# Kernel tuning notes

Measured on AMD Instinct MI355X. Metric: run time of the kernel, lower is better.

## Reference

```python
import jax, jax.numpy as jnp
import numpy as np

D_MODEL = 2048
NUM_HEADS = 32
NUM_KV_HEADS = 8
HEAD_DIM = D_MODEL // NUM_HEADS
ROPE_BASE = 10000.0


def _rope_cos_sin(T, dtype):
    # standard LLaMA-style RoPE tables, shape (1, 1, T, head_dim)
    half = HEAD_DIM // 2
    inv_freq = 1.0 / (ROPE_BASE ** (jnp.arange(0, half, dtype=jnp.float32) / half))
    pos = jnp.arange(T, dtype=jnp.float32)
    freqs = pos[:, None] * inv_freq[None, :]          # (T, half)
    emb = jnp.concatenate([freqs, freqs], axis=-1)     # (T, head_dim)
    cos = jnp.cos(emb)[None, None].astype(dtype)
    sin = jnp.sin(emb)[None, None].astype(dtype)
    return cos, sin


def _rotate_half(x):
    h = x.shape[-1] // 2
    return jnp.concatenate([-x[..., h:], x[..., :h]], axis=-1)


def setup_inputs() -> dict:
    key = jax.random.key(0)
    ks = jax.random.split(key, 5)
    B, T = 2, 2048
    s = 1.0 / np.sqrt(D_MODEL)
    return {
        "x": jax.random.normal(ks[0], (B, T, D_MODEL), jnp.float32),
        "Wq": jax.random.normal(ks[1], (D_MODEL, D_MODEL), jnp.float32) * s,
        "Wk": jax.random.normal(ks[2], (NUM_KV_HEADS * HEAD_DIM, D_MODEL), jnp.float32) * s,
        "Wv": jax.random.normal(ks[3], (NUM_KV_HEADS * HEAD_DIM, D_MODEL), jnp.float32) * s,
        "Wo": jax.random.normal(ks[4], (D_MODEL, D_MODEL), jnp.float32) * s,
    }


def reference(x, Wq, Wk, Wv, Wo):
    B, T, _ = x.shape
    # projections (torch Linear: y = x @ W.T)
    Q = (x @ Wq.T).reshape(B, T, NUM_HEADS, HEAD_DIM).transpose(0, 2, 1, 3)      # (B,H,T,D)
    K = (x @ Wk.T).reshape(B, T, NUM_KV_HEADS, HEAD_DIM).transpose(0, 2, 1, 3)   # (B,Hkv,T,D)
    V = (x @ Wv.T).reshape(B, T, NUM_KV_HEADS, HEAD_DIM).transpose(0, 2, 1, 3)

    cos, sin = _rope_cos_sin(T, x.dtype)
    Q = Q * cos + _rotate_half(Q) * sin
    K = K * cos + _rotate_half(K) * sin

    # GQA: expand kv heads to query heads
    heads_per_kv = NUM_HEADS // NUM_KV_HEADS
    group_map = jnp.arange(NUM_HEADS) // heads_per_kv
    K_sel = K[:, group_map]  # (B,H,T,D)
    V_sel = V[:, group_map]

    scale = 1.0 / np.sqrt(HEAD_DIM)
    scores = jnp.einsum("bhqd,bhkd->bhqk", Q, K_sel) * scale
    causal = jnp.tril(jnp.ones((T, T), dtype=bool))
    scores = jnp.where(causal, scores, jnp.finfo(scores.dtype).min)
    attn = jax.nn.softmax(scores, axis=-1)
    out = jnp.einsum("bhqk,bhkd->bhqd", attn, V_sel)
    out = out.transpose(0, 2, 1, 3).reshape(B, T, D_MODEL)
    return out @ Wo.T
```

## Files before the change

### kernel.cpp

```cpp
#include <hip/hip_runtime.h>
#include <stdint.h>


typedef unsigned short u16;
typedef __attribute__((ext_vector_type(8))) short short8;
typedef __attribute__((ext_vector_type(4))) float floatx4;

#define T_SEQ 2048
#define DMODEL 2048
#define NHEADS 32
#define KVHEADS 8
#define HDIM 64
#define QK_SCALE 0.1803368801111204f

__device__ __forceinline__ u16 f2bf(float f) {
  uint32_t u = __builtin_bit_cast(uint32_t, f);
  u = (u + 0x7FFFu + ((u >> 16) & 1u)) >> 16;
  return (u16)u;
}
__device__ __forceinline__ float bf2f(u16 h) {
  uint32_t u = ((uint32_t)h) << 16;
  return __builtin_bit_cast(float, u);
}
__device__ __forceinline__ uint32_t cvtpk(float a, float b) {
  uint32_t r;
  asm("v_cvt_pk_bf16_f32 %0, %1, %2" : "=v"(r) : "v"(a), "v"(b));
  return r;
}

__device__ __forceinline__ void gld_lds16(const void* g, void* l) {
  __builtin_amdgcn_global_load_lds(
      (const __attribute__((address_space(1))) unsigned int*)g,
      (__attribute__((address_space(3))) unsigned int*)l, 16, 0, 0);
}

__global__ __launch_bounds__(256) void cvt_kernel(const float* __restrict__ src,
                                                  u16* __restrict__ dst, int n4) {
  int i = blockIdx.x * 256 + threadIdx.x;
  if (i >= n4) return;
  float4 v = ((const float4*)src)[i];
  ushort4 o;
  o.x = f2bf(v.x); o.y = f2bf(v.y); o.z = f2bf(v.z); o.w = f2bf(v.w);
  ((ushort4*)dst)[i] = o;
}

__global__ __launch_bounds__(256) void rope_table_kernel(float* __restrict__ cosT,
                                                         float* __restrict__ sinT) {
  int idx = blockIdx.x * 256 + threadIdx.x;
  int t = idx >> 5, i = idx & 31;
  float invf = 1.0f / powf(10000.0f, (float)i / 32.0f);
  float a = (float)t * invf;
  cosT[idx] = cosf(a);
  sinT[idx] = sinf(a);
}

template <bool OUT_F32>
__global__ __launch_bounds__(256) void gemm_bt(const u16* __restrict__ A,
                                               const u16* __restrict__ Bm,
                                               float* __restrict__ Cf,
                                               u16* __restrict__ Cb,
                                               int M, int N, int K) {
  __shared__ u16 As[128 * 64];
  __shared__ u16 Bs[128 * 64];
  const int tid = threadIdx.x;
  const int lane = tid & 63;
  const int wid = tid >> 6;
  const int wr = wid >> 1, wc = wid & 1;
  const long bm = (long)blockIdx.y * 128;
  const long bn = (long)blockIdx.x * 128;

  floatx4 acc[4][4] = {};

  for (int kt = 0; kt < K; kt += 64) {
#pragma unroll
    for (int c = 0; c < 4; ++c) {
      int g = (wid * 4 + c) * 64 + lane;
      int row = g >> 3, slot = g & 7;
      int ss = slot ^ (row & 7);
      gld_lds16(A + (bm + row) * (long)K + kt + ss * 8, (char*)As + g * 16);
      gld_lds16(Bm + (bn + row) * (long)K + kt + ss * 8, (char*)Bs + g * 16);
    }
    __syncthreads();
#pragma unroll
    for (int ks = 0; ks < 2; ++ks) {
      short8 af[4], bfr[4];
#pragma unroll
      for (int m = 0; m < 4; ++m) {
        int row = wr * 64 + m * 16 + (lane & 15);
        int slot = (ks * 4 + (lane >> 4)) ^ (row & 7);
        af[m] = *(const short8*)((const char*)As + row * 128 + slot * 16);
      }
#pragma unroll
      for (int n = 0; n < 4; ++n) {
        int row = wc * 64 + n * 16 + (lane & 15);
        int slot = (ks * 4 + (lane >> 4)) ^ (row & 7);
        bfr[n] = *(const short8*)((const char*)Bs + row * 128 + slot * 16);
      }
#pragma unroll
      for (int m = 0; m < 4; ++m)
#pragma unroll
        for (int n = 0; n < 4; ++n)
          acc[m][n] = __builtin_amdgcn_mfma_f32_16x16x32_bf16(af[m], bfr[n],
                                                              acc[m][n], 0, 0, 0);
    }
    __syncthreads();
  }
#pragma unroll
  for (int m = 0; m < 4; ++m)
#pragma unroll
    for (int n = 0; n < 4; ++n)
#pragma unroll
      for (int r = 0; r < 4; ++r) {
        long row = bm + wr * 64 + m * 16 + (lane >> 4) * 4 + r;
        long col = bn + wc * 64 + n * 16 + (lane & 15);
        if constexpr (OUT_F32)
          Cf[row * N + col] = acc[m][n][r];
        else
          Cb[row * N + col] = f2bf(acc[m][n][r]);
      }
}

__global__ __launch_bounds__(256) void rope_apply_kernel(
    const u16* __restrict__ QKV, const float* __restrict__ cosT,
    const float* __restrict__ sinT, u16* __restrict__ Qh, u16* __restrict__ Kh) {
  int idx = blockIdx.x * 256 + threadIdx.x;
  int c = idx % 2560;
  int bt = idx / 2560;
  int t = bt & (T_SEQ - 1);
  int b = bt >> 11;
  int hd = c & 63;
  int i = hd & 31;
  float cs = cosT[t * 32 + i];
  float sn = sinT[t * 32 + i];
  long base = (long)bt * 3072;
  float xv = bf2f(QKV[base + c]);
  int pairc = (hd < 32) ? c + 32 : c - 32;
  float xp = bf2f(QKV[base + pairc]);
  float rot = (hd < 32) ? -xp : xp;
  float ov = xv * cs + rot * sn;
  if (c < 2048) {
    int h = c >> 6;
    Qh[((long)(b * NHEADS + h) * T_SEQ + t) * HDIM + hd] = f2bf(ov * QK_SCALE);
  } else {
    int kv = (c - 2048) >> 6;
    Kh[((long)(b * KVHEADS + kv) * T_SEQ + t) * HDIM + hd] = f2bf(ov);
  }
}

__global__ __launch_bounds__(256) void v_transpose_kernel(const u16* __restrict__ QKV,
                                                          u16* __restrict__ Vt) {
  __shared__ u16 tl[64 * 65];
  int blk = blockIdx.x;
  int ttile = blk & 31;
  int kvh = (blk >> 5) & 7;
  int b = blk >> 8;
  int tid = threadIdx.x;
  long bt0 = (long)b * T_SEQ + ttile * 64;
#pragma unroll
  for (int j = 0; j < 2; ++j) {
    int chunk = tid * 2 + j;
    int el = chunk * 8;
    int row = el >> 6, col = el & 63;
    short8 v = *(const short8*)(QKV + (bt0 + row) * 3072 + 2560 + kvh * 64 + col);
#pragma unroll
    for (int k = 0; k < 8; ++k) tl[(col + k) * 65 + row] = (u16)v[k];
  }
  __syncthreads();
#pragma unroll
  for (int j = 0; j < 2; ++j) {
    int chunk = tid * 2 + j;
    int el = chunk * 8;
    int d = el >> 6, t0 = el & 63;
    short8 o;
#pragma unroll
    for (int k = 0; k < 8; ++k) o[k] = (short)tl[d * 65 + t0 + k];
    *(short8*)(Vt + ((long)(b * KVHEADS + kvh) * HDIM + d) * T_SEQ + ttile * 64 + t0) = o;
  }
}

#define ATT_BODY(BUF)                                                          \
  {                                                                            \
    asm volatile("s_waitcnt vmcnt(0)" ::: "memory");                           \
    __builtin_amdgcn_s_barrier();                                              \
    asm volatile("" ::: "memory");                                             \
    if (kt < qb) {                                                             \
      gld_lds16(kg0, (char*)KS + ((BUF ^ 1) * 8192) + ld0);                    \
      gld_lds16(kg1, (char*)KS + ((BUF ^ 1) * 8192) + ld1);                    \
      gld_lds16(vg0, (char*)VS + ((BUF ^ 1) * 8192) + ld0);                    \
      gld_lds16(vg1, (char*)VS + ((BUF ^ 1) * 8192) + ld1);                    \
      kg0 += 4096; kg1 += 4096; vg0 += 64; vg1 += 64;                          \
    }                                                                          \
    floatx4 st[4] = {};                                                        \
    __builtin_amdgcn_s_setprio(1);                                             \
    {                                                                          \
      short8 kf0 = *(const short8*)((const char*)KS + BUF * 8192 + aK0);       \
      short8 kf1 = *(const short8*)((const char*)KS + BUF * 8192 + aK0 + 2048);\
      short8 kf2 = *(const short8*)((const char*)KS + BUF * 8192 + aK0 + 4096);\
      short8 kf3 = *(const short8*)((const char*)KS + BUF * 8192 + aK0 + 6144);\
      st[0] = __builtin_amdgcn_mfma_f32_16x16x32_bf16(kf0, qf0, st[0], 0, 0, 0);\
      st[1] = __builtin_amdgcn_mfma_f32_16x16x32_bf16(kf1, qf0, st[1], 0, 0, 0);\
      st[2] = __builtin_amdgcn_mfma_f32_16x16x32_bf16(kf2, qf0, st[2], 0, 0, 0);\
      st[3] = __builtin_amdgcn_mfma_f32_16x16x32_bf16(kf3, qf0, st[3], 0, 0, 0);\
      kf0 = *(const short8*)((const char*)KS + BUF * 8192 + aK1);              \
      kf1 = *(const short8*)((const char*)KS + BUF * 8192 + aK1 + 2048);       \
      kf2 = *(const short8*)((const char*)KS + BUF * 8192 + aK1 + 4096);       \
      kf3 = *(const short8*)((const char*)KS + BUF * 8192 + aK1 + 6144);       \
      st[0] = __builtin_amdgcn_mfma_f32_16x16x32_bf16(kf0, qf1, st[0], 0, 0, 0);\
      st[1] = __builtin_amdgcn_mfma_f32_16x16x32_bf16(kf1, qf1, st[1], 0, 0, 0);\
      st[2] = __builtin_amdgcn_mfma_f32_16x16x32_bf16(kf2, qf1, st[2], 0, 0, 0);\
      st[3] = __builtin_amdgcn_mfma_f32_16x16x32_bf16(kf3, qf1, st[3], 0, 0, 0);\
    }                                                                          \
    __builtin_amdgcn_s_setprio(0);                                             \
    if (kt == qb) {                                                            \
      _Pragma("unroll") for (int tt = 0; tt < 4; ++tt)                         \
        _Pragma("unroll") for (int r = 0; r < 4; ++r) {                        \
          int tg = kt * 64 + tt * 16 + l4 * 4 + r;                             \
          if (tg > qg) st[tt][r] = -1e30f;                                     \
        }                                                                      \
    }                                                                          \
    float mx0 = fmaxf(fmaxf(st[0][0], st[0][1]), fmaxf(st[0][2], st[0][3]));   \
    float mx1 = fmaxf(fmaxf(st[1][0], st[1][1]), fmaxf(st[1][2], st[1][3]));   \
    float mx2 = fmaxf(fmaxf(st[2][0], st[2][1]), fmaxf(st[2][2], st[2][3]));   \
    float mx3 = fmaxf(fmaxf(st[3][0], st[3][1]), fmaxf(st[3][2], st[3][3]));   \
    float mt = fmaxf(fmaxf(mx0, mx1), fmaxf(mx2, mx3));                        \
    mt = fmaxf(mt, __shfl_xor(mt, 16));                                        \
    mt = fmaxf(mt, __shfl_xor(mt, 32));                                        \
    bool defer = __all(mt - m_run <= 8.0f);                                    \
    float m_use = defer ? m_run : fmaxf(m_run, mt);                            \
    float alpha = defer ? 1.0f : exp2f(m_run - m_use);                         \
    float lsp[4];                                                              \
    _Pragma("unroll") for (int tt = 0; tt < 4; ++tt) {                         \
      float e0 = exp2f(st[tt][0] - m_use);                                     \
      float e1 = exp2f(st[tt][1] - m_use);                                     \
      float e2 = exp2f(st[tt][2] - m_use);                                     \
      float e3 = exp2f(st[tt][3] - m_use);                                     \
      st[tt][0] = e0; st[tt][1] = e1;                                          \
      lsp[tt] = (e0 + e1) + (e2 + e3);                                         \
      uint2 pk;                                                                \
      pk.x = cvtpk(e0, e1);                                                    \
      pk.y = cvtpk(e2, e3);                                                    \
      *(uint2*)((char*)Ps + (pwb ^ (tt << 5))) = pk;                           \
    }                                                                          \
    float lsum = (lsp[0] + lsp[1]) + (lsp[2] + lsp[3]);                        \
    lsum += __shfl_xor(lsum, 16);                                              \
    lsum += __shfl_xor(lsum, 32);                                              \
    l_run = l_run * alpha + lsum;                                              \
    m_run = m_use;                                                             \
    if (!defer) {                                                              \
      float a0 = __shfl(alpha, l4 * 4 + 0);                                    \
      float a1 = __shfl(alpha, l4 * 4 + 1);                                    \
      float a2 = __shfl(alpha, l4 * 4 + 2);                                    \
      float a3 = __shfl(alpha, l4 * 4 + 3);                                    \
      _Pragma("unroll") for (int dd = 0; dd < 4; ++dd) {                       \
        oA[dd][0] *= a0; oA[dd][1] *= a1; oA[dd][2] *= a2; oA[dd][3] *= a3;    \
      }                                                                        \
    }                                                                          \
    asm volatile("s_waitcnt lgkmcnt(0)" ::: "memory");                         \
    __builtin_amdgcn_s_setprio(1);                                             \
    {                                                                          \
      short8 pa = *(const short8*)((const char*)Ps + pr0);                     \
      short8 vb0 = *(const short8*)((const char*)VS + BUF * 8192 + aK0);       \
      short8 vb1 = *(const short8*)((const char*)VS + BUF * 8192 + aK0 + 2048);\
      short8 vb2 = *(const short8*)((const char*)VS + BUF * 8192 + aK0 + 4096);\
      short8 vb3 = *(const short8*)((const char*)VS + BUF * 8192 + aK0 + 6144);\
      oA[0] = __builtin_amdgcn_mfma_f32_16x16x32_bf16(pa, vb0, oA[0], 0, 0, 0);\
      oA[1] = __builtin_amdgcn_mfma_f32_16x16x32_bf16(pa, vb1, oA[1], 0, 0, 0);\
      oA[2] = __builtin_amdgcn_mfma_f32_16x16x32_bf16(pa, vb2, oA[2], 0, 0, 0);\
      oA[3] = __builtin_amdgcn_mfma_f32_16x16x32_bf16(pa, vb3, oA[3], 0, 0, 0);\
      pa = *(const short8*)((const char*)Ps + pr1);                            \
      vb0 = *(const short8*)((const char*)VS + BUF * 8192 + aK1);              \
      vb1 = *(const short8*)((const char*)VS + BUF * 8192 + aK1 + 2048);       \
      vb2 = *(const short8*)((const char*)VS + BUF * 8192 + aK1 + 4096);       \
      vb3 = *(const short8*)((const char*)VS + BUF * 8192 + aK1 + 6144);       \
      oA[0] = __builtin_amdgcn_mfma_f32_16x16x32_bf16(pa, vb0, oA[0], 0, 0, 0);\
      oA[1] = __builtin_amdgcn_mfma_f32_16x16x32_bf16(pa, vb1, oA[1], 0, 0, 0);\
      oA[2] = __builtin_amdgcn_mfma_f32_16x16x32_bf16(pa, vb2, oA[2], 0, 0, 0);\
      oA[3] = __builtin_amdgcn_mfma_f32_16x16x32_bf16(pa, vb3, oA[3], 0, 0, 0);\
    }                                                                          \
    __builtin_amdgcn_s_setprio(0);                                             \
  }

__global__ __launch_bounds__(256, 4) void attn_kernel(const u16* __restrict__ Qh,
                                                      const u16* __restrict__ Kh,
                                                      const u16* __restrict__ Vt,
                                                      u16* __restrict__ O) {
  __shared__ u16 KS[2][4096];
  __shared__ u16 VS[2][4096];
  __shared__ u16 Ps[4 * 1024];
  const int tid = threadIdx.x;
  const int lane = tid & 63;
  const int w = tid >> 6;
  const int blk = blockIdx.x;
  const int qb = 31 - (blk & 31);
  const int h = (blk >> 5) & 31;
  const int b = blk >> 10;
  const int kvh = h >> 2;
  const int qbase = qb * 64;
  const int l15 = lane & 15;
  const int l4 = lane >> 4;

  const u16* Qp = Qh + ((long)(b * NHEADS + h) * T_SEQ + qbase + w * 16 + l15) * HDIM;
  const short8 qf0 = *(const short8*)(Qp + l4 * 8);
  const short8 qf1 = *(const short8*)(Qp + 32 + l4 * 8);
  const u16* Kbase = Kh + (long)(b * KVHEADS + kvh) * T_SEQ * HDIM;
  const u16* Vbase = Vt + (long)(b * KVHEADS + kvh) * HDIM * T_SEQ;

  const int aK0 = l15 * 128 + ((l4 ^ (l15 & 7)) << 4);
  const int aK1 = l15 * 128 + (((4 + l4) ^ (l15 & 7)) << 4);
  const int pwb = w * 2048 + l15 * 128 + ((((l4 >> 1) ^ (l15 & 7))) << 4) + (l4 & 1) * 8;
  const int pr0 = w * 2048 + aK0;
  const int pr1 = w * 2048 + aK1;

  int g0 = (w * 2 + 0) * 64 + lane, g1 = (w * 2 + 1) * 64 + lane;
  int r0 = g0 >> 3, s0g = (g0 & 7) ^ (r0 & 7);
  int r1 = g1 >> 3, s1g = (g1 & 7) ^ (r1 & 7);
  const int ld0 = g0 * 16, ld1 = g1 * 16;
  const u16* kg0 = Kbase + r0 * HDIM + s0g * 8;
  const u16* kg1 = Kbase + r1 * HDIM + s1g * 8;
  const u16* vg0 = Vbase + r0 * T_SEQ + s0g * 8;
  const u16* vg1 = Vbase + r1 * T_SEQ + s1g * 8;

  float m_run = -1e30f, l_run = 0.f;
  floatx4 oA[4] = {};
  const int qg = qbase + w * 16 + l15;

  gld_lds16(kg0, (char*)KS + ld0);
  gld_lds16(kg1, (char*)KS + ld1);
  gld_lds16(vg0, (char*)VS + ld0);
  gld_lds16(vg1, (char*)VS + ld1);
  kg0 += 4096; kg1 += 4096; vg0 += 64; vg1 += 64;

  int kt = 0;
  for (;;) {
    ATT_BODY(0);
    if (kt >= qb) break;
    ++kt;
    ATT_BODY(1);
    if (kt >= qb) break;
    ++kt;
  }

  float linv = 1.0f / l_run;
  float i0 = __shfl(linv, l4 * 4 + 0);
  float i1 = __shfl(linv, l4 * 4 + 1);
  float i2 = __shfl(linv, l4 * 4 + 2);
  float i3 = __shfl(linv, l4 * 4 + 3);
  float iv[4] = {i0, i1, i2, i3};
#pragma unroll
  for (int dd = 0; dd < 4; ++dd)
#pragma unroll
    for (int r = 0; r < 4; ++r) {
      int trow = qbase + w * 16 + l4 * 4 + r;
      int col = h * 64 + dd * 16 + l15;
      O[((long)b * T_SEQ + trow) * DMODEL + col] = f2bf(oA[dd][r] * iv[r]);
    }
}

extern "C" void kernel_launch(void* const* d_in, const int* in_sizes, int n_in,
                              void* d_out, int out_size, void* d_ws, size_t ws_size,
                              hipStream_t stream) {
  const float* x = (const float*)d_in[0];
  const float* Wq = (const float*)d_in[1];
  const float* Wk = (const float*)d_in[2];
  const float* Wv = (const float*)d_in[3];
  const float* Wo = (const float*)d_in[4];
  float* out = (float*)d_out;

  char* ws = (char*)d_ws;
  u16* x_bf = (u16*)(ws);
  u16* Obuf = (u16*)(ws);
  u16* Wqkv_bf = (u16*)(ws + 16777216);
  u16* Wo_bf = (u16*)(ws + 29360128);
  u16* QKV = (u16*)(ws + 37748736);
  u16* Qh = (u16*)(ws + 62914560);
  u16* Kh = (u16*)(ws + 79691776);
  u16* Vt = (u16*)(ws + 83886080);
  float* cosT = (float*)(ws + 88080384);
  float* sinT = (float*)(ws + 88342528);

  cvt_kernel<<<8192, 256, 0, stream>>>(x, x_bf, 2097152);
  cvt_kernel<<<4096, 256, 0, stream>>>(Wq, Wqkv_bf, 1048576);
  cvt_kernel<<<1024, 256, 0, stream>>>(Wk, Wqkv_bf + 2048 * 2048, 262144);
  cvt_kernel<<<1024, 256, 0, stream>>>(Wv, Wqkv_bf + 2560 * 2048, 262144);
  cvt_kernel<<<4096, 256, 0, stream>>>(Wo, Wo_bf, 1048576);
  rope_table_kernel<<<256, 256, 0, stream>>>(cosT, sinT);

  dim3 g1(24, 32);
  gemm_bt<false><<<g1, 256, 0, stream>>>(x_bf, Wqkv_bf, nullptr, QKV, 4096, 3072, 2048);

  rope_apply_kernel<<<40960, 256, 0, stream>>>(QKV, cosT, sinT, Qh, Kh);
  v_transpose_kernel<<<512, 256, 0, stream>>>(QKV, Vt);

  attn_kernel<<<2048, 256, 0, stream>>>(Qh, Kh, Vt, Obuf);

  dim3 g2(16, 32);
  gemm_bt<true><<<g2, 256, 0, stream>>>(Obuf, Wo_bf, out, nullptr, 4096, 2048, 2048);
}
```

Baseline: 371.6 us.

## Process 128 query rows per attention block, two 16-row tiles per wave

The attention kernel now gives each block 128 query rows instead of 64, so each wave computes two 16-row Q tiles (A and B) against every K/V tile it loads into LDS. This halves the number of K/V loads into shared memory per query row and halves the grid. In exchange it adds redundant work on the diagonal tiles, uses more registers and LDS (occupancy hint lowered from 4 to 3), and makes the causal load imbalance coarser. A single running max is shared by both row sets within a wave.

```diff
diff --git a/kernel.cpp b/kernel.cpp
--- a/kernel.cpp
+++ b/kernel.cpp
@@ -183,68 +183,91 @@
     asm volatile("s_waitcnt vmcnt(0)" ::: "memory");                           \
     __builtin_amdgcn_s_barrier();                                              \
     asm volatile("" ::: "memory");                                             \
-    if (kt < qb) {                                                             \
+    if (kt < ktmax) {                                                          \
       gld_lds16(kg0, (char*)KS + ((BUF ^ 1) * 8192) + ld0);                    \
       gld_lds16(kg1, (char*)KS + ((BUF ^ 1) * 8192) + ld1);                    \
       gld_lds16(vg0, (char*)VS + ((BUF ^ 1) * 8192) + ld0);                    \
       gld_lds16(vg1, (char*)VS + ((BUF ^ 1) * 8192) + ld1);                    \
       kg0 += 4096; kg1 += 4096; vg0 += 64; vg1 += 64;                          \
     }                                                                          \
-    floatx4 st[4] = {};                                                        \
+    floatx4 stA[4] = {}, stB[4] = {};                                          \
     __builtin_amdgcn_s_setprio(1);                                             \
     {                                                                          \
       short8 kf0 = *(const short8*)((const char*)KS + BUF * 8192 + aK0);       \
       short8 kf1 = *(const short8*)((const char*)KS + BUF * 8192 + aK0 + 2048);\
       short8 kf2 = *(const short8*)((const char*)KS + BUF * 8192 + aK0 + 4096);\
       short8 kf3 = *(const short8*)((const char*)KS + BUF * 8192 + aK0 + 6144);\
-      st[0] = __builtin_amdgcn_mfma_f32_16x16x32_bf16(kf0, qf0, st[0], 0, 0, 0);\
-      st[1] = __builtin_amdgcn_mfma_f32_16x16x32_bf16(kf1, qf0, st[1], 0, 0, 0);\
-      st[2] = __builtin_amdgcn_mfma_f32_16x16x32_bf16(kf2, qf0, st[2], 0, 0, 0);\
-      st[3] = __builtin_amdgcn_mfma_f32_16x16x32_bf16(kf3, qf0, st[3], 0, 0, 0);\
+      stA[0] = __builtin_amdgcn_mfma_f32_16x16x32_bf16(kf0, qfA0, stA[0], 0, 0, 0);\
+      stB[0] = __builtin_amdgcn_mfma_f32_16x16x32_bf16(kf0, qfB0, stB[0], 0, 0, 0);\
+      stA[1] = __builtin_amdgcn_mfma_f32_16x16x32_bf16(kf1, qfA0, stA[1], 0, 0, 0);\
+      stB[1] = __builtin_amdgcn_mfma_f32_16x16x32_bf16(kf1, qfB0, stB[1], 0, 0, 0);\
+      stA[2] = __builtin_amdgcn_mfma_f32_16x16x32_bf16(kf2, qfA0, stA[2], 0, 0, 0);\
+      stB[2] = __builtin_amdgcn_mfma_f32_16x16x32_bf16(kf2, qfB0, stB[2], 0, 0, 0);\
+      stA[3] = __builtin_amdgcn_mfma_f32_16x16x32_bf16(kf3, qfA0, stA[3], 0, 0, 0);\
+      stB[3] = __builtin_amdgcn_mfma_f32_16x16x32_bf16(kf3, qfB0, stB[3], 0, 0, 0);\
       kf0 = *(const short8*)((const char*)KS + BUF * 8192 + aK1);              \
       kf1 = *(const short8*)((const char*)KS + BUF * 8192 + aK1 + 2048);       \
       kf2 = *(const short8*)((const char*)KS + BUF * 8192 + aK1 + 4096);       \
       kf3 = *(const short8*)((const char*)KS + BUF * 8192 + aK1 + 6144);       \
-      st[0] = __builtin_amdgcn_mfma_f32_16x16x32_bf16(kf0, qf1, st[0], 0, 0, 0);\
-      st[1] = __builtin_amdgcn_mfma_f32_16x16x32_bf16(kf1, qf1, st[1], 0, 0, 0);\
-      st[2] = __builtin_amdgcn_mfma_f32_16x16x32_bf16(kf2, qf1, st[2], 0, 0, 0);\
-      st[3] = __builtin_amdgcn_mfma_f32_16x16x32_bf16(kf3, qf1, st[3], 0, 0, 0);\
+      stA[0] = __builtin_amdgcn_mfma_f32_16x16x32_bf16(kf0, qfA1, stA[0], 0, 0, 0);\
+      stB[0] = __builtin_amdgcn_mfma_f32_16x16x32_bf16(kf0, qfB1, stB[0], 0, 0, 0);\
+      stA[1] = __builtin_amdgcn_mfma_f32_16x16x32_bf16(kf1, qfA1, stA[1], 0, 0, 0);\
+      stB[1] = __builtin_amdgcn_mfma_f32_16x16x32_bf16(kf1, qfB1, stB[1], 0, 0, 0);\
+      stA[2] = __builtin_amdgcn_mfma_f32_16x16x32_bf16(kf2, qfA1, stA[2], 0, 0, 0);\
+      stB[2] = __builtin_amdgcn_mfma_f32_16x16x32_bf16(kf2, qfB1, stB[2], 0, 0, 0);\
+      stA[3] = __builtin_amdgcn_mfma_f32_16x16x32_bf16(kf3, qfA1, stA[3], 0, 0, 0);\
+      stB[3] = __builtin_amdgcn_mfma_f32_16x16x32_bf16(kf3, qfB1, stB[3], 0, 0, 0);\
     }                                                                          \
     __builtin_amdgcn_s_setprio(0);                                             \
-    if (kt == qb) {                                                            \
+    if (kt >= dt) {                                                            \
       _Pragma("unroll") for (int tt = 0; tt < 4; ++tt)                         \
         _Pragma("unroll") for (int r = 0; r < 4; ++r) {                        \
           int tg = kt * 64 + tt * 16 + l4 * 4 + r;                             \
-          if (tg > qg) st[tt][r] = -1e30f;                                     \
+          if (tg > qgA) stA[tt][r] = -1e30f;                                   \
+          if (tg > qgB) stB[tt][r] = -1e30f;                                   \
         }                                                                      \
     }                                                                          \
-    float mx0 = fmaxf(fmaxf(st[0][0], st[0][1]), fmaxf(st[0][2], st[0][3]));   \
-    float mx1 = fmaxf(fmaxf(st[1][0], st[1][1]), fmaxf(st[1][2], st[1][3]));   \
-    float mx2 = fmaxf(fmaxf(st[2][0], st[2][1]), fmaxf(st[2][2], st[2][3]));   \
-    float mx3 = fmaxf(fmaxf(st[3][0], st[3][1]), fmaxf(st[3][2], st[3][3]));   \
-    float mt = fmaxf(fmaxf(mx0, mx1), fmaxf(mx2, mx3));                        \
+    float mxA0 = fmaxf(fmaxf(stA[0][0], stA[0][1]), fmaxf(stA[0][2], stA[0][3]));\
+    float mxA1 = fmaxf(fmaxf(stA[1][0], stA[1][1]), fmaxf(stA[1][2], stA[1][3]));\
+    float mxA2 = fmaxf(fmaxf(stA[2][0], stA[2][1]), fmaxf(stA[2][2], stA[2][3]));\
+    float mxA3 = fmaxf(fmaxf(stA[3][0], stA[3][1]), fmaxf(stA[3][2], stA[3][3]));\
+    float mxB0 = fmaxf(fmaxf(stB[0][0], stB[0][1]), fmaxf(stB[0][2], stB[0][3]));\
+    float mxB1 = fmaxf(fmaxf(stB[1][0], stB[1][1]), fmaxf(stB[1][2], stB[1][3]));\
+    float mxB2 = fmaxf(fmaxf(stB[2][0], stB[2][1]), fmaxf(stB[2][2], stB[2][3]));\
+    float mxB3 = fmaxf(fmaxf(stB[3][0], stB[3][1]), fmaxf(stB[3][2], stB[3][3]));\
+    float mt = fmaxf(fmaxf(fmaxf(mxA0, mxA1), fmaxf(mxA2, mxA3)),              \
+                     fmaxf(fmaxf(mxB0, mxB1), fmaxf(mxB2, mxB3)));             \
     mt = fmaxf(mt, __shfl_xor(mt, 16));                                        \
     mt = fmaxf(mt, __shfl_xor(mt, 32));                                        \
     bool defer = __all(mt - m_run <= 8.0f);                                    \
     float m_use = defer ? m_run : fmaxf(m_run, mt);                            \
     float alpha = defer ? 1.0f : exp2f(m_run - m_use);                         \
-    float lsp[4];                                                              \
+    float lsA = 0.f, lsB = 0.f;                                                \
     _Pragma("unroll") for (int tt = 0; tt < 4; ++tt) {                         \
-      float e0 = exp2f(st[tt][0] - m_use);                                     \
-      float e1 = exp2f(st[tt][1] - m_use);                                     \
-      float e2 = exp2f(st[tt][2] - m_use);                                     \
-      float e3 = exp2f(st[tt][3] - m_use);                                     \
-      st[tt][0] = e0; st[tt][1] = e1;                                          \
-      lsp[tt] = (e0 + e1) + (e2 + e3);                                         \
+      float e0 = exp2f(stA[tt][0] - m_use);                                    \
+      float e1 = exp2f(stA[tt][1] - m_use);                                    \
+      float e2 = exp2f(stA[tt][2] - m_use);                                    \
+      float e3 = exp2f(stA[tt][3] - m_use);                                    \
+      lsA += (e0 + e1) + (e2 + e3);                                            \
       uint2 pk;                                                                \
       pk.x = cvtpk(e0, e1);                                                    \
       pk.y = cvtpk(e2, e3);                                                    \
-      *(uint2*)((char*)Ps + (pwb ^ (tt << 5))) = pk;                           \
-    }                                                                          \
-    float lsum = (lsp[0] + lsp[1]) + (lsp[2] + lsp[3]);                        \
-    lsum += __shfl_xor(lsum, 16);                                              \
-    lsum += __shfl_xor(lsum, 32);                                              \
-    l_run = l_run * alpha + lsum;                                              \
+      *(uint2*)((char*)Ps + (pwbA ^ (tt << 5))) = pk;                          \
+      float f0 = exp2f(stB[tt][0] - m_use);                                    \
+      float f1 = exp2f(stB[tt][1] - m_use);                                    \
+      float f2 = exp2f(stB[tt][2] - m_use);                                    \
+      float f3 = exp2f(stB[tt][3] - m_use);                                    \
+      lsB += (f0 + f1) + (f2 + f3);                                            \
+      pk.x = cvtpk(f0, f1);                                                    \
+      pk.y = cvtpk(f2, f3);                                                    \
+      *(uint2*)((char*)Ps + (pwbB ^ (tt << 5))) = pk;                          \
+    }                                                                          \
+    lsA += __shfl_xor(lsA, 16);                                                \
+    lsA += __shfl_xor(lsA, 32);                                                \
+    lsB += __shfl_xor(lsB, 16);                                                \
+    lsB += __shfl_xor(lsB, 32);                                                \
+    l_runA = l_runA * alpha + lsA;                                             \
+    l_runB = l_runB * alpha + lsB;                                             \
     m_run = m_use;                                                             \
     if (!defer) {                                                              \
       float a0 = __shfl(alpha, l4 * 4 + 0);                                    \
@@ -253,63 +276,81 @@
       float a3 = __shfl(alpha, l4 * 4 + 3);                                    \
       _Pragma("unroll") for (int dd = 0; dd < 4; ++dd) {                       \
         oA[dd][0] *= a0; oA[dd][1] *= a1; oA[dd][2] *= a2; oA[dd][3] *= a3;    \
+        oB[dd][0] *= a0; oB[dd][1] *= a1; oB[dd][2] *= a2; oB[dd][3] *= a3;    \
       }                                                                        \
     }                                                                          \
     asm volatile("s_waitcnt lgkmcnt(0)" ::: "memory");                         \
     __builtin_amdgcn_s_setprio(1);                                             \
     {                                                                          \
-      short8 pa = *(const short8*)((const char*)Ps + pr0);                     \
+      short8 paA = *(const short8*)((const char*)Ps + prA0);                   \
+      short8 paB = *(const short8*)((const char*)Ps + prB0);                   \
       short8 vb0 = *(const short8*)((const char*)VS + BUF * 8192 + aK0);       \
       short8 vb1 = *(const short8*)((const char*)VS + BUF * 8192 + aK0 + 2048);\
       short8 vb2 = *(const short8*)((const char*)VS + BUF * 8192 + aK0 + 4096);\
       short8 vb3 = *(const short8*)((const char*)VS + BUF * 8192 + aK0 + 6144);\
-      oA[0] = __builtin_amdgcn_mfma_f32_16x16x32_bf16(pa, vb0, oA[0], 0, 0, 0);\
-      oA[1] = __builtin_amdgcn_mfma_f32_16x16x32_bf16(pa, vb1, oA[1], 0, 0, 0);\
-      oA[2] = __builtin_amdgcn_mfma_f32_16x16x32_bf16(pa, vb2, oA[2], 0, 0, 0);\
-      oA[3] = __builtin_amdgcn_mfma_f32_16x16x32_bf16(pa, vb3, oA[3], 0, 0, 0);\
-      pa = *(const short8*)((const char*)Ps + pr1);                            \
+      oA[0] = __builtin_amdgcn_mfma_f32_16x16x32_bf16(paA, vb0, oA[0], 0, 0, 0);\
+      oB[0] = __builtin_amdgcn_mfma_f32_16x16x32_bf16(paB, vb0, oB[0], 0, 0, 0);\
+      oA[1] = __builtin_amdgcn_mfma_f32_16x16x32_bf16(paA, vb1, oA[1], 0, 0, 0);\
+      oB[1] = __builtin_amdgcn_mfma_f32_16x16x32_bf16(paB, vb1, oB[1], 0, 0, 0);\
+      oA[2] = __builtin_amdgcn_mfma_f32_16x16x32_bf16(paA, vb2, oA[2], 0, 0, 0);\
+      oB[2] = __builtin_amdgcn_mfma_f32_16x16x32_bf16(paB, vb2, oB[2], 0, 0, 0);\
+      oA[3] = __builtin_amdgcn_mfma_f32_16x16x32_bf16(paA, vb3, oA[3], 0, 0, 0);\
+      oB[3] = __builtin_amdgcn_mfma_f32_16x16x32_bf16(paB, vb3, oB[3], 0, 0, 0);\
+      paA = *(const short8*)((const char*)Ps + prA1);                          \
+      paB = *(const short8*)((const char*)Ps + prB1);                          \
       vb0 = *(const short8*)((const char*)VS + BUF * 8192 + aK1);              \
       vb1 = *(const short8*)((const char*)VS + BUF * 8192 + aK1 + 2048);       \
       vb2 = *(const short8*)((const char*)VS + BUF * 8192 + aK1 + 4096);       \
       vb3 = *(const short8*)((const char*)VS + BUF * 8192 + aK1 + 6144);       \
-      oA[0] = __builtin_amdgcn_mfma_f32_16x16x32_bf16(pa, vb0, oA[0], 0, 0, 0);\
-      oA[1] = __builtin_amdgcn_mfma_f32_16x16x32_bf16(pa, vb1, oA[1], 0, 0, 0);\
-      oA[2] = __builtin_amdgcn_mfma_f32_16x16x32_bf16(pa, vb2, oA[2], 0, 0, 0);\
-      oA[3] = __builtin_amdgcn_mfma_f32_16x16x32_bf16(pa, vb3, oA[3], 0, 0, 0);\
+      oA[0] = __builtin_amdgcn_mfma_f32_16x16x32_bf16(paA, vb0, oA[0], 0, 0, 0);\
+      oB[0] = __builtin_amdgcn_mfma_f32_16x16x32_bf16(paB, vb0, oB[0], 0, 0, 0);\
+      oA[1] = __builtin_amdgcn_mfma_f32_16x16x32_bf16(paA, vb1, oA[1], 0, 0, 0);\
+      oB[1] = __builtin_amdgcn_mfma_f32_16x16x32_bf16(paB, vb1, oB[1], 0, 0, 0);\
+      oA[2] = __builtin_amdgcn_mfma_f32_16x16x32_bf16(paA, vb2, oA[2], 0, 0, 0);\
+      oB[2] = __builtin_amdgcn_mfma_f32_16x16x32_bf16(paB, vb2, oB[2], 0, 0, 0);\
+      oA[3] = __builtin_amdgcn_mfma_f32_16x16x32_bf16(paA, vb3, oA[3], 0, 0, 0);\
+      oB[3] = __builtin_amdgcn_mfma_f32_16x16x32_bf16(paB, vb3, oB[3], 0, 0, 0);\
     }                                                                          \
     __builtin_amdgcn_s_setprio(0);                                             \
   }
 
-__global__ __launch_bounds__(256, 4) void attn_kernel(const u16* __restrict__ Qh,
+__global__ __launch_bounds__(256, 3) void attn_kernel(const u16* __restrict__ Qh,
                                                       const u16* __restrict__ Kh,
                                                       const u16* __restrict__ Vt,
                                                       u16* __restrict__ O) {
   __shared__ u16 KS[2][4096];
   __shared__ u16 VS[2][4096];
-  __shared__ u16 Ps[4 * 1024];
+  __shared__ u16 Ps[4 * 2048];
   const int tid = threadIdx.x;
   const int lane = tid & 63;
   const int w = tid >> 6;
   const int blk = blockIdx.x;
-  const int qb = 31 - (blk & 31);
-  const int h = (blk >> 5) & 31;
-  const int b = blk >> 10;
+  const int qbi = 15 - (blk & 15);
+  const int h = (blk >> 4) & 31;
+  const int b = blk >> 9;
   const int kvh = h >> 2;
-  const int qbase = qb * 64;
+  const int qbase = qbi * 128;
   const int l15 = lane & 15;
   const int l4 = lane >> 4;
-
-  const u16* Qp = Qh + ((long)(b * NHEADS + h) * T_SEQ + qbase + w * 16 + l15) * HDIM;
-  const short8 qf0 = *(const short8*)(Qp + l4 * 8);
-  const short8 qf1 = *(const short8*)(Qp + 32 + l4 * 8);
+  const int ktmax = 2 * qbi + 1;
+  const int dt = 2 * qbi + (w >> 1);
+
+  const u16* Qp = Qh + ((long)(b * NHEADS + h) * T_SEQ + qbase + w * 32 + l15) * HDIM;
+  const short8 qfA0 = *(const short8*)(Qp + l4 * 8);
+  const short8 qfA1 = *(const short8*)(Qp + 32 + l4 * 8);
+  const short8 qfB0 = *(const short8*)(Qp + 16 * HDIM + l4 * 8);
+  const short8 qfB1 = *(const short8*)(Qp + 16 * HDIM + 32 + l4 * 8);
   const u16* Kbase = Kh + (long)(b * KVHEADS + kvh) * T_SEQ * HDIM;
   const u16* Vbase = Vt + (long)(b * KVHEADS + kvh) * HDIM * T_SEQ;
 
   const int aK0 = l15 * 128 + ((l4 ^ (l15 & 7)) << 4);
   const int aK1 = l15 * 128 + (((4 + l4) ^ (l15 & 7)) << 4);
-  const int pwb = w * 2048 + l15 * 128 + ((((l4 >> 1) ^ (l15 & 7))) << 4) + (l4 & 1) * 8;
-  const int pr0 = w * 2048 + aK0;
-  const int pr1 = w * 2048 + aK1;
+  const int pwbA = w * 4096 + l15 * 128 + ((((l4 >> 1) ^ (l15 & 7))) << 4) + (l4 & 1) * 8;
+  const int pwbB = pwbA + 2048;
+  const int prA0 = w * 4096 + aK0;
+  const int prA1 = w * 4096 + aK1;
+  const int prB0 = prA0 + 2048;
+  const int prB1 = prA1 + 2048;
 
   int g0 = (w * 2 + 0) * 64 + lane, g1 = (w * 2 + 1) * 64 + lane;
   int r0 = g0 >> 3, s0g = (g0 & 7) ^ (r0 & 7);
@@ -320,9 +361,10 @@
   const u16* vg0 = Vbase + r0 * T_SEQ + s0g * 8;
   const u16* vg1 = Vbase + r1 * T_SEQ + s1g * 8;
 
-  float m_run = -1e30f, l_run = 0.f;
-  floatx4 oA[4] = {};
-  const int qg = qbase + w * 16 + l15;
+  float m_run = -1e30f, l_runA = 0.f, l_runB = 0.f;
+  floatx4 oA[4] = {}, oB[4] = {};
+  const int qgA = qbase + w * 32 + l15;
+  const int qgB = qgA + 16;
 
   gld_lds16(kg0, (char*)KS + ld0);
   gld_lds16(kg1, (char*)KS + ld1);
@@ -333,26 +375,33 @@
   int kt = 0;
   for (;;) {
     ATT_BODY(0);
-    if (kt >= qb) break;
+    if (kt >= ktmax) break;
     ++kt;
     ATT_BODY(1);
-    if (kt >= qb) break;
+    if (kt >= ktmax) break;
     ++kt;
   }
 
-  float linv = 1.0f / l_run;
-  float i0 = __shfl(linv, l4 * 4 + 0);
-  float i1 = __shfl(linv, l4 * 4 + 1);
-  float i2 = __shfl(linv, l4 * 4 + 2);
-  float i3 = __shfl(linv, l4 * 4 + 3);
-  float iv[4] = {i0, i1, i2, i3};
+  float linvA = 1.0f / l_runA;
+  float linvB = 1.0f / l_runB;
+  float iA0 = __shfl(linvA, l4 * 4 + 0);
+  float iA1 = __shfl(linvA, l4 * 4 + 1);
+  float iA2 = __shfl(linvA, l4 * 4 + 2);
+  float iA3 = __shfl(linvA, l4 * 4 + 3);
+  float iB0 = __shfl(linvB, l4 * 4 + 0);
+  float iB1 = __shfl(linvB, l4 * 4 + 1);
+  float iB2 = __shfl(linvB, l4 * 4 + 2);
+  float iB3 = __shfl(linvB, l4 * 4 + 3);
+  float ivA[4] = {iA0, iA1, iA2, iA3};
+  float ivB[4] = {iB0, iB1, iB2, iB3};
 #pragma unroll
   for (int dd = 0; dd < 4; ++dd)
 #pragma unroll
     for (int r = 0; r < 4; ++r) {
-      int trow = qbase + w * 16 + l4 * 4 + r;
+      int trowA = qbase + w * 32 + l4 * 4 + r;
       int col = h * 64 + dd * 16 + l15;
-      O[((long)b * T_SEQ + trow) * DMODEL + col] = f2bf(oA[dd][r] * iv[r]);
+      O[((long)b * T_SEQ + trowA) * DMODEL + col] = f2bf(oA[dd][r] * ivA[r]);
+      O[((long)b * T_SEQ + trowA + 16) * DMODEL + col] = f2bf(oB[dd][r] * ivB[r]);
     }
 }
 
@@ -391,7 +440,7 @@
   rope_apply_kernel<<<40960, 256, 0, stream>>>(QKV, cosT, sinT, Qh, Kh);
   v_transpose_kernel<<<512, 256, 0, stream>>>(QKV, Vt);
 
-  attn_kernel<<<2048, 256, 0, stream>>>(Qh, Kh, Vt, Obuf);
+  attn_kernel<<<1024, 256, 0, stream>>>(Qh, Kh, Vt, Obuf);
 
   dim3 g2(16, 32);
   gemm_bt<true><<<g2, 256, 0, stream>>>(Obuf, Wo_bf, out, nullptr, 4096, 2048, 2048);
```

New measurement: 369.1 us. Within noise of the previous version (-0.7%).
